# Performance work log

Hardware: AMD Instinct MI355X
Metric: run time of the kernel (lower is better)

## Reference

```python
import jax, jax.numpy as jnp
import numpy as np

N, IN, H, C, E = 20000, 256, 256, 16, 640000

def sage_conv(x, edge_index, W_l, b_l, W_r):
    # PyG SAGEConv (aggr='mean', root_weight=True):
    # out = lin_l(mean_{j in N(i)} x_j) + lin_r(x_i)
    src, dst = edge_index[0], edge_index[1]
    n = x.shape[0]
    msgs = x[src]                                            # [E, d] irregular gather
    agg = jax.ops.segment_sum(msgs, dst, num_segments=n)     # [N, d]
    deg = jax.ops.segment_sum(jnp.ones((msgs.shape[0],), x.dtype), dst, num_segments=n)
    agg = agg / jnp.maximum(deg, 1.0)[:, None]               # mean aggregation
    return agg @ W_l + b_l + x @ W_r


def setup_inputs() -> dict:
    key = jax.random.key(0)
    ks = jax.random.split(key, 10)
    s = lambda k, fi, fo: jax.random.normal(k, (fi, fo), jnp.float32) / np.sqrt(fi)
    return {
        "x": jax.random.normal(ks[0], (N, IN), jnp.float32),
        "edge_index": jax.random.randint(ks[1], (2, E), 0, N, jnp.int64),
        "W1l": s(ks[2], IN, H), "b1": jnp.zeros((H,), jnp.float32), "W1r": s(ks[3], IN, H),
        "W2l": s(ks[4], H, H),  "b2": jnp.zeros((H,), jnp.float32), "W2r": s(ks[5], H, H),
        "Wc": s(ks[6], H, C),   "bc": jnp.zeros((C,), jnp.float32),
    }


def reference(x, edge_index, W1l, b1, W1r, W2l, b2, W2r, Wc, bc):
    h = sage_conv(x, edge_index, W1l, b1, W1r)
    h = jax.nn.relu(h)                    # dropout is identity in eval mode
    z = sage_conv(h, edge_index, W2l, b2, W2r)
    return z @ Wc + bc                    # classifier logits [N, C]
```

## Files before the change

### kernel.cpp

```cpp
#include <hip/hip_runtime.h>
#include <hip/hip_bf16.h>


#define FEAT 256
#define NCLS 16
#define ZPAD 264
#define CAP  128

typedef __bf16 bf16x8 __attribute__((ext_vector_type(8)));
typedef __bf16 bf16x4 __attribute__((ext_vector_type(4)));
typedef float  f32x4  __attribute__((ext_vector_type(4)));
typedef float  f32x2  __attribute__((ext_vector_type(2)));
typedef unsigned int uint4v __attribute__((ext_vector_type(4)));

#define ACC8(S, U) do {                                                   \
    _Pragma("unroll")                                                     \
    for (int w_ = 0; w_ < 4; ++w_) {                                      \
        f32x2 lo_ = __builtin_amdgcn_cvt_pk_f32_fp8(U[w_], false);        \
        f32x2 hi_ = __builtin_amdgcn_cvt_pk_f32_fp8(U[w_], true);         \
        S[w_][0] += lo_[0]; S[w_][1] += lo_[1];                           \
        S[w_][2] += hi_[0]; S[w_][3] += hi_[1];                           \
    } } while (0)


__global__ void combo_kernel(const float* __restrict__ x,
                             const float* __restrict__ W1l, const float* __restrict__ W1r,
                             const float* __restrict__ W2l, const float* __restrict__ W2r,
                             const float* __restrict__ Wc, const float* __restrict__ b2,
                             const float* __restrict__ bc,
                             const int* __restrict__ src, const int* __restrict__ dst,
                             __bf16* __restrict__ xb, unsigned char* __restrict__ x8,
                             __bf16* __restrict__ W1lT, __bf16* __restrict__ W1rT,
                             __bf16* __restrict__ WaT, __bf16* __restrict__ WbT,
                             float* __restrict__ bc2,
                             int* __restrict__ cnt, unsigned short* __restrict__ bucket,
                             int n4, int E, int nb_edge, int nb_cvt) {
    int t = threadIdx.x;
    int bx = blockIdx.x;
    if (bx < nb_edge) {
        int e4 = (bx * 256 + t) * 4;
        if (((E & 3) == 0) && e4 + 3 < E) {
            int4 sv = *(const int4*)(src + e4);
            int4 dv = *(const int4*)(dst + e4);
            int p0 = atomicAdd(&cnt[dv.x], 1);
            int p1 = atomicAdd(&cnt[dv.y], 1);
            int p2 = atomicAdd(&cnt[dv.z], 1);
            int p3 = atomicAdd(&cnt[dv.w], 1);
            if (p0 < CAP) __builtin_nontemporal_store((unsigned short)sv.x, &bucket[(size_t)dv.x * CAP + p0]);
            if (p1 < CAP) __builtin_nontemporal_store((unsigned short)sv.y, &bucket[(size_t)dv.y * CAP + p1]);
            if (p2 < CAP) __builtin_nontemporal_store((unsigned short)sv.z, &bucket[(size_t)dv.z * CAP + p2]);
            if (p3 < CAP) __builtin_nontemporal_store((unsigned short)sv.w, &bucket[(size_t)dv.w * CAP + p3]);
        } else {
            for (int k = 0; k < 4 && e4 + k < E; ++k) {
                int s = src[e4 + k], d = dst[e4 + k];
                int p = atomicAdd(&cnt[d], 1);
                if (p < CAP) __builtin_nontemporal_store((unsigned short)s, &bucket[(size_t)d * CAP + p]);
            }
        }
    } else if (bx < nb_edge + nb_cvt) {
        int i = (bx - nb_edge) * 256 + t;
        if (i < n4) {
            f32x4 v = ((const f32x4*)x)[i];
            bf16x4 o;
            #pragma unroll
            for (int j = 0; j < 4; ++j) o[j] = (__bf16)v[j];
            ((bf16x4*)xb)[i] = o;
            int pk = 0;
            pk = __builtin_amdgcn_cvt_pk_fp8_f32(v[0], v[1], pk, false);
            pk = __builtin_amdgcn_cvt_pk_fp8_f32(v[2], v[3], pk, true);
            ((int*)x8)[i] = pk;
        }
    } else if (bx < nb_edge + nb_cvt + 512) {
        int b = bx - nb_edge - nb_cvt;
        int w = b >> 8, nn = b & 255;
        const float* W = w ? W1r : W1l;
        __bf16* WT = w ? W1rT : W1lT;
        WT[nn * FEAT + t] = (__bf16)W[t * FEAT + nn];
    } else if (bx < nb_edge + nb_cvt + 512 + 32) {
        int b = bx - nb_edge - nb_cvt - 512;
        int c = b & 15;
        const float* W = (b < 16) ? W2l : W2r;
        __bf16* WT = (b < 16) ? WaT : WbT;
        float s = 0.f;
        #pragma unroll 4
        for (int m = 0; m < FEAT; ++m)
            s += W[t * FEAT + m] * Wc[m * NCLS + c];
        WT[c * FEAT + t] = (__bf16)s;
    } else {
        if (t < NCLS) {
            float s = 0.f;
            for (int k = 0; k < FEAT; ++k) s += b2[k] * Wc[k * NCLS + t];
            bc2[t] = s + bc[t];
        }
    }
}


__global__ __launch_bounds__(256) void agg_fp8_kernel(
    const unsigned char* __restrict__ t8, const int* __restrict__ cnt,
    const unsigned short* __restrict__ bucket, __bf16* __restrict__ out, int n)
{
    int wave = threadIdx.x >> 6;
    int node = blockIdx.x * 4 + wave;
    if (node >= n) return;
    int lane = threadIdx.x & 63;
    int quad = lane >> 4, l16 = lane & 15;
    int c = cnt[node];
    int deg = c < CAP ? c : CAP;
    const unsigned short* lst = bucket + node * CAP;

    int e0 = 0, e1 = 0;
    if (lane < deg)      e0 = lst[lane];
    if (lane + 64 < deg) e1 = lst[lane + 64];

    f32x4 s0[4], s1[4];
    #pragma unroll
    for (int w = 0; w < 4; ++w) { s0[w] = (f32x4){0.f,0.f,0.f,0.f}; s1[w] = (f32x4){0.f,0.f,0.f,0.f}; }

    int nfull = deg >> 2;
    int rem   = deg & 3;
    const unsigned char* base = t8 + l16 * 16;

    int tt = 0;
    for (; tt + 3 < nfull; tt += 4) {
        int i0 = (tt + 0) * 4 + quad, i1 = (tt + 1) * 4 + quad;
        int i2 = (tt + 2) * 4 + quad, i3 = (tt + 3) * 4 + quad;
        int j0 = (i0 < 64) ? __shfl(e0, i0) : __shfl(e1, i0 - 64);
        int j1 = (i1 < 64) ? __shfl(e0, i1) : __shfl(e1, i1 - 64);
        int j2 = (i2 < 64) ? __shfl(e0, i2) : __shfl(e1, i2 - 64);
        int j3 = (i3 < 64) ? __shfl(e0, i3) : __shfl(e1, i3 - 64);
        uint4v u0 = *(const uint4v*)(base + (size_t)j0 * FEAT);
        uint4v u1 = *(const uint4v*)(base + (size_t)j1 * FEAT);
        uint4v u2 = *(const uint4v*)(base + (size_t)j2 * FEAT);
        uint4v u3 = *(const uint4v*)(base + (size_t)j3 * FEAT);
        ACC8(s0, u0); ACC8(s1, u1); ACC8(s0, u2); ACC8(s1, u3);
    }
    for (; tt < nfull; ++tt) {
        int i = tt * 4 + quad;
        int j = (i < 64) ? __shfl(e0, i) : __shfl(e1, i - 64);
        uint4v u = *(const uint4v*)(base + (size_t)j * FEAT);
        ACC8(s0, u);
    }
    if (rem) {
        int i = nfull * 4 + quad;
        int j = (i < 64) ? __shfl(e0, i) : __shfl(e1, i - 64);
        if (quad < rem) {
            uint4v u = *(const uint4v*)(base + (size_t)j * FEAT);
            ACC8(s1, u);
        }
    }

    #pragma unroll
    for (int w = 0; w < 4; ++w)
        #pragma unroll
        for (int j = 0; j < 4; ++j) {
            float v = s0[w][j] + s1[w][j];
            v += __shfl_xor(v, 16, 64);
            v += __shfl_xor(v, 32, 64);
            s0[w][j] = v;
        }

    float inv = (c > 0) ? 1.0f / (float)c : 0.0f;
    bf16x4 o;
    #pragma unroll
    for (int j = 0; j < 4; ++j) o[j] = (__bf16)(s0[quad][j] * inv);
    *(bf16x4*)(out + (size_t)node * FEAT + l16 * 16 + quad * 4) = o;
}


__global__ __launch_bounds__(256) void gemm1_kernel(
    const __bf16* __restrict__ A1, const __bf16* __restrict__ A2,
    const __bf16* __restrict__ B1T, const __bf16* __restrict__ B2T,
    const float* __restrict__ bias,
    const __bf16* __restrict__ WaT, const __bf16* __restrict__ WbT,
    const float* __restrict__ bc2,
    __bf16* __restrict__ pb, float* __restrict__ q, int M)
{
    __shared__ __align__(16) __bf16 tile[32][ZPAD];

    int m0   = blockIdx.x * 32;
    int lane = threadIdx.x & 63;
    int wave = threadIdx.x >> 6;
    int l16  = lane & 15, quad = lane >> 4;

    f32x4 acc[2][4];
    #pragma unroll
    for (int a = 0; a < 2; ++a)
        #pragma unroll
        for (int b = 0; b < 4; ++b) acc[a][b] = (f32x4){0.f, 0.f, 0.f, 0.f};

    int arow[2];
    #pragma unroll
    for (int mt = 0; mt < 2; ++mt) {
        int r = m0 + mt * 16 + l16;
        arow[mt] = (r < M) ? r : (M - 1);
    }
    int nbase = wave * 64;

    for (int pass = 0; pass < 2; ++pass) {
        const __bf16* A  = pass ? A2 : A1;
        const __bf16* BT = pass ? B2T : B1T;
        #pragma unroll 2
        for (int kk = 0; kk < 8; ++kk) {
            int k0 = kk * 32 + quad * 8;
            bf16x8 af[2], bfm[4];
            #pragma unroll
            for (int mt = 0; mt < 2; ++mt)
                af[mt] = *(const bf16x8*)(A + (size_t)arow[mt] * FEAT + k0);
            #pragma unroll
            for (int nt = 0; nt < 4; ++nt)
                bfm[nt] = *(const bf16x8*)(BT + (size_t)(nbase + nt * 16 + l16) * FEAT + k0);
            #pragma unroll
            for (int mt = 0; mt < 2; ++mt)
                #pragma unroll
                for (int nt = 0; nt < 4; ++nt)
                    acc[mt][nt] = __builtin_amdgcn_mfma_f32_16x16x32_bf16(
                        af[mt], bfm[nt], acc[mt][nt], 0, 0, 0);
        }
    }

    #pragma unroll
    for (int nt = 0; nt < 4; ++nt) {
        int col = nbase + nt * 16 + l16;
        float bv = bias[col];
        #pragma unroll
        for (int mt = 0; mt < 2; ++mt) {
            int lr = mt * 16 + quad * 4;
            #pragma unroll
            for (int r = 0; r < 4; ++r) {
                float v = acc[mt][nt][r] + bv;
                tile[lr + r][col] = (__bf16)(v > 0.f ? v : 0.f);
            }
        }
    }
    __syncthreads();

    {
        int half = wave >> 1;
        int lr = half * 16 + l16;
        const __bf16* WT = (wave & 1) ? WbT : WaT;
        f32x4 a = {0.f, 0.f, 0.f, 0.f};
        #pragma unroll
        for (int kk = 0; kk < 8; ++kk) {
            int k0 = kk * 32 + quad * 8;
            bf16x8 av = *(const bf16x8*)(&tile[lr][k0]);
            bf16x8 bv = *(const bf16x8*)(WT + (size_t)l16 * FEAT + k0);
            a = __builtin_amdgcn_mfma_f32_16x16x32_bf16(av, bv, a, 0, 0, 0);
        }
        if (wave & 1) {
            float qv = bc2[l16];
            #pragma unroll
            for (int r = 0; r < 4; ++r) {
                int row = m0 + half * 16 + quad * 4 + r;
                if (row < M) q[(size_t)row * NCLS + l16] = a[r] + qv;
            }
        } else {
            #pragma unroll
            for (int r = 0; r < 4; ++r) {
                int row = m0 + half * 16 + quad * 4 + r;
                if (row < M) pb[(size_t)row * NCLS + l16] = (__bf16)a[r];
            }
        }
    }
}


__global__ __launch_bounds__(256) void agg_out_kernel(
    const __bf16* __restrict__ pb, const float* __restrict__ q,
    const int* __restrict__ cnt, const unsigned short* __restrict__ bucket,
    float* __restrict__ out, int n)
{
    int wave = threadIdx.x >> 6;
    int node = blockIdx.x * 4 + wave;
    if (node >= n) return;
    int lane = threadIdx.x & 63;
    int quad = lane >> 4, l16 = lane & 15;
    int c = cnt[node];
    int deg = c < CAP ? c : CAP;
    const unsigned short* lst = bucket + node * CAP;

    int e0 = 0, e1 = 0;
    if (lane < deg)      e0 = lst[lane];
    if (lane + 64 < deg) e1 = lst[lane + 64];

    float s0 = 0.f, s1 = 0.f;
    int nfull = deg >> 2;
    int rem   = deg & 3;

    int tt = 0;
    for (; tt + 3 < nfull; tt += 4) {
        int i0 = (tt + 0) * 4 + quad, i1 = (tt + 1) * 4 + quad;
        int i2 = (tt + 2) * 4 + quad, i3 = (tt + 3) * 4 + quad;
        int j0 = (i0 < 64) ? __shfl(e0, i0) : __shfl(e1, i0 - 64);
        int j1 = (i1 < 64) ? __shfl(e0, i1) : __shfl(e1, i1 - 64);
        int j2 = (i2 < 64) ? __shfl(e0, i2) : __shfl(e1, i2 - 64);
        int j3 = (i3 < 64) ? __shfl(e0, i3) : __shfl(e1, i3 - 64);
        float v0 = (float)pb[(size_t)j0 * NCLS + l16];
        float v1 = (float)pb[(size_t)j1 * NCLS + l16];
        float v2 = (float)pb[(size_t)j2 * NCLS + l16];
        float v3 = (float)pb[(size_t)j3 * NCLS + l16];
        s0 += v0 + v1;
        s1 += v2 + v3;
    }
    for (; tt < nfull; ++tt) {
        int i = tt * 4 + quad;
        int j = (i < 64) ? __shfl(e0, i) : __shfl(e1, i - 64);
        s0 += (float)pb[(size_t)j * NCLS + l16];
    }
    if (rem) {
        int i = nfull * 4 + quad;
        int j = (i < 64) ? __shfl(e0, i) : __shfl(e1, i - 64);
        if (quad < rem) s1 += (float)pb[(size_t)j * NCLS + l16];
    }

    float v = s0 + s1;
    v += __shfl_xor(v, 16, 64);
    v += __shfl_xor(v, 32, 64);

    if (quad == 0) {
        float inv = (c > 0) ? 1.0f / (float)c : 0.0f;
        out[(size_t)node * NCLS + l16] = v * inv + q[(size_t)node * NCLS + l16];
    }
}


extern "C" void kernel_launch(void* const* d_in, const int* in_sizes, int n_in,
                              void* d_out, int out_size, void* d_ws, size_t ws_size,
                              hipStream_t stream) {
    const float* x   = (const float*)d_in[0];
    const int*   ei  = (const int*)d_in[1];
    const float* W1l = (const float*)d_in[2];
    const float* b1  = (const float*)d_in[3];
    const float* W1r = (const float*)d_in[4];
    const float* W2l = (const float*)d_in[5];
    const float* b2  = (const float*)d_in[6];
    const float* W2r = (const float*)d_in[7];
    const float* Wc  = (const float*)d_in[8];
    const float* bc  = (const float*)d_in[9];
    float* out = (float*)d_out;

    const int n = in_sizes[0] / FEAT;
    const int E = in_sizes[1] / 2;
    const int* srcp = ei;
    const int* dstp = ei + E;

    char* p = (char*)d_ws;
    auto alloc = [&](size_t bytes) { char* r = p; p += (bytes + 511) & ~511ull; return r; };
    int* cnt       = (int*)alloc((size_t)n * 4);
    unsigned short* bucket = (unsigned short*)alloc((size_t)n * CAP * 2);
    __bf16* W1lT   = (__bf16*)alloc((size_t)FEAT * FEAT * 2);
    __bf16* W1rT   = (__bf16*)alloc((size_t)FEAT * FEAT * 2);
    __bf16* WaT    = (__bf16*)alloc((size_t)NCLS * FEAT * 2);
    __bf16* WbT    = (__bf16*)alloc((size_t)NCLS * FEAT * 2);
    float*  bc2    = (float*)alloc((size_t)NCLS * 4);
    __bf16* xb     = (__bf16*)alloc((size_t)n * FEAT * 2);
    unsigned char* x8 = (unsigned char*)alloc((size_t)n * FEAT);
    __bf16* aggb   = (__bf16*)alloc((size_t)n * FEAT * 2);
    __bf16* pb     = (__bf16*)alloc((size_t)n * NCLS * 2);
    float*  qb     = (float*)alloc((size_t)n * NCLS * 4);

    int n4 = n * FEAT / 4;
    int nb_cvt  = (n4 + 255) / 256;
    int nb_edge = (E + 1023) / 1024;

    hipMemsetAsync(cnt, 0, (size_t)n * 4, stream);

    combo_kernel<<<nb_edge + nb_cvt + 512 + 32 + 1, 256, 0, stream>>>(
        x, W1l, W1r, W2l, W2r, Wc, b2, bc, srcp, dstp,
        xb, x8, W1lT, W1rT, WaT, WbT, bc2, cnt, bucket, n4, E, nb_edge, nb_cvt);

    agg_fp8_kernel<<<(n + 3) / 4, 256, 0, stream>>>(x8, cnt, bucket, aggb, n);
    gemm1_kernel<<<(n + 31) / 32, 256, 0, stream>>>(aggb, xb, W1lT, W1rT, b1,
                                                    WaT, WbT, bc2, pb, qb, n);

    agg_out_kernel<<<(n + 3) / 4, 256, 0, stream>>>(pb, qb, cnt, bucket, out, n);
}
```

Before: 214.0 us.

## Shard per-node edge bucket counters across eight sub-buckets to reduce atomic contention

The CSR-like bucket build now splits each destination node's counter and slot list into 8 shards chosen by block index, so concurrent atomics on the same node land on different addresses. The edge blocks move to the end of the combo kernel and handle 2 edges per thread instead of 4. The aggregation kernels rebuild a compacted neighbour list from the shard counts with a small unrolled prefix walk. In exchange, counter memory grows 8x and bucket memory 4x (larger memset and more scattered stores), and each aggregation wave does extra per-lane index arithmetic.

```diff
diff --git a/kernel.cpp b/kernel.cpp
--- a/kernel.cpp
+++ b/kernel.cpp
@@ -5,7 +5,10 @@
 #define FEAT 256
 #define NCLS 16
 #define ZPAD 264
-#define CAP  128
+#define NSH  8
+#define SCAP 64
+#define SLOTS (NSH * SCAP)
+#define CAPTOT 128
 
 typedef __bf16 bf16x8 __attribute__((ext_vector_type(8)));
 typedef __bf16 bf16x4 __attribute__((ext_vector_type(4)));
@@ -21,6 +24,36 @@
         S[w_][0] += lo_[0]; S[w_][1] += lo_[1];                           \
         S[w_][2] += hi_[0]; S[w_][3] += hi_[1];                           \
     } } while (0)
+
+__device__ __forceinline__ void load_entries(
+    const int* __restrict__ cnt, const unsigned short* __restrict__ bucket,
+    int node, int lane, int& e0, int& e1, int& deg, float& inv)
+{
+    int4 ca = *(const int4*)(cnt + node * NSH);
+    int4 cb = *(const int4*)(cnt + node * NSH + 4);
+    int cs[NSH] = {ca.x, ca.y, ca.z, ca.w, cb.x, cb.y, cb.z, cb.w};
+    int ctrue = 0, d = 0;
+    #pragma unroll
+    for (int s = 0; s < NSH; ++s) {
+        ctrue += cs[s];
+        cs[s] = cs[s] < SCAP ? cs[s] : SCAP;
+        d += cs[s];
+    }
+    deg = d < CAPTOT ? d : CAPTOT;
+    inv = ctrue > 0 ? 1.0f / (float)ctrue : 0.0f;
+    const unsigned short* lst = bucket + (size_t)node * SLOTS;
+
+    auto get = [&](int i) -> int {
+        int s = 0, loc = i;
+        #pragma unroll
+        for (int t = 0; t < NSH - 1; ++t) {
+            if (s == t && loc >= cs[t]) { loc -= cs[t]; s = t + 1; }
+        }
+        return lst[s * SCAP + loc];
+    };
+    e0 = (lane < deg)      ? get(lane)      : 0;
+    e1 = (lane + 64 < deg) ? get(lane + 64) : 0;
+}
 
 
 __global__ void combo_kernel(const float* __restrict__ x,
@@ -34,31 +67,11 @@
                              __bf16* __restrict__ WaT, __bf16* __restrict__ WbT,
                              float* __restrict__ bc2,
                              int* __restrict__ cnt, unsigned short* __restrict__ bucket,
-                             int n4, int E, int nb_edge, int nb_cvt) {
+                             int n4, int E, int nb_cvt) {
     int t = threadIdx.x;
     int bx = blockIdx.x;
-    if (bx < nb_edge) {
-        int e4 = (bx * 256 + t) * 4;
-        if (((E & 3) == 0) && e4 + 3 < E) {
-            int4 sv = *(const int4*)(src + e4);
-            int4 dv = *(const int4*)(dst + e4);
-            int p0 = atomicAdd(&cnt[dv.x], 1);
-            int p1 = atomicAdd(&cnt[dv.y], 1);
-            int p2 = atomicAdd(&cnt[dv.z], 1);
-            int p3 = atomicAdd(&cnt[dv.w], 1);
-            if (p0 < CAP) __builtin_nontemporal_store((unsigned short)sv.x, &bucket[(size_t)dv.x * CAP + p0]);
-            if (p1 < CAP) __builtin_nontemporal_store((unsigned short)sv.y, &bucket[(size_t)dv.y * CAP + p1]);
-            if (p2 < CAP) __builtin_nontemporal_store((unsigned short)sv.z, &bucket[(size_t)dv.z * CAP + p2]);
-            if (p3 < CAP) __builtin_nontemporal_store((unsigned short)sv.w, &bucket[(size_t)dv.w * CAP + p3]);
-        } else {
-            for (int k = 0; k < 4 && e4 + k < E; ++k) {
-                int s = src[e4 + k], d = dst[e4 + k];
-                int p = atomicAdd(&cnt[d], 1);
-                if (p < CAP) __builtin_nontemporal_store((unsigned short)s, &bucket[(size_t)d * CAP + p]);
-            }
-        }
-    } else if (bx < nb_edge + nb_cvt) {
-        int i = (bx - nb_edge) * 256 + t;
+    if (bx < nb_cvt) {
+        int i = bx * 256 + t;
         if (i < n4) {
             f32x4 v = ((const f32x4*)x)[i];
             bf16x4 o;
@@ -70,14 +83,14 @@
             pk = __builtin_amdgcn_cvt_pk_fp8_f32(v[2], v[3], pk, true);
             ((int*)x8)[i] = pk;
         }
-    } else if (bx < nb_edge + nb_cvt + 512) {
-        int b = bx - nb_edge - nb_cvt;
+    } else if (bx < nb_cvt + 512) {
+        int b = bx - nb_cvt;
         int w = b >> 8, nn = b & 255;
         const float* W = w ? W1r : W1l;
         __bf16* WT = w ? W1rT : W1lT;
         WT[nn * FEAT + t] = (__bf16)W[t * FEAT + nn];
-    } else if (bx < nb_edge + nb_cvt + 512 + 32) {
-        int b = bx - nb_edge - nb_cvt - 512;
+    } else if (bx < nb_cvt + 512 + 32) {
+        int b = bx - nb_cvt - 512;
         int c = b & 15;
         const float* W = (b < 16) ? W2l : W2r;
         __bf16* WT = (b < 16) ? WaT : WbT;
@@ -86,11 +99,25 @@
         for (int m = 0; m < FEAT; ++m)
             s += W[t * FEAT + m] * Wc[m * NCLS + c];
         WT[c * FEAT + t] = (__bf16)s;
-    } else {
+    } else if (bx == nb_cvt + 512 + 32) {
         if (t < NCLS) {
             float s = 0.f;
             for (int k = 0; k < FEAT; ++k) s += b2[k] * Wc[k * NCLS + t];
             bc2[t] = s + bc[t];
+        }
+    } else {
+        int sh = bx & (NSH - 1);
+        int idx = (bx - nb_cvt - 512 - 33) * 256 + t;
+        int e2 = idx * 2;
+        if (e2 < E) {
+            int2 sv = *(const int2*)(src + e2);
+            int2 dv = *(const int2*)(dst + e2);
+            int p0 = atomicAdd(&cnt[dv.x * NSH + sh], 1);
+            if (p0 < SCAP) bucket[(size_t)dv.x * SLOTS + sh * SCAP + p0] = (unsigned short)sv.x;
+            if (e2 + 1 < E) {
+                int p1 = atomicAdd(&cnt[dv.y * NSH + sh], 1);
+                if (p1 < SCAP) bucket[(size_t)dv.y * SLOTS + sh * SCAP + p1] = (unsigned short)sv.y;
+            }
         }
     }
 }
@@ -105,13 +132,9 @@
     if (node >= n) return;
     int lane = threadIdx.x & 63;
     int quad = lane >> 4, l16 = lane & 15;
-    int c = cnt[node];
-    int deg = c < CAP ? c : CAP;
-    const unsigned short* lst = bucket + node * CAP;
-
-    int e0 = 0, e1 = 0;
-    if (lane < deg)      e0 = lst[lane];
-    if (lane + 64 < deg) e1 = lst[lane + 64];
+
+    int e0, e1, deg; float inv;
+    load_entries(cnt, bucket, node, lane, e0, e1, deg, inv);
 
     f32x4 s0[4], s1[4];
     #pragma unroll
@@ -160,7 +183,6 @@
             s0[w][j] = v;
         }
 
-    float inv = (c > 0) ? 1.0f / (float)c : 0.0f;
     bf16x4 o;
     #pragma unroll
     for (int j = 0; j < 4; ++j) o[j] = (__bf16)(s0[quad][j] * inv);
@@ -275,13 +297,9 @@
     if (node >= n) return;
     int lane = threadIdx.x & 63;
     int quad = lane >> 4, l16 = lane & 15;
-    int c = cnt[node];
-    int deg = c < CAP ? c : CAP;
-    const unsigned short* lst = bucket + node * CAP;
-
-    int e0 = 0, e1 = 0;
-    if (lane < deg)      e0 = lst[lane];
-    if (lane + 64 < deg) e1 = lst[lane + 64];
+
+    int e0, e1, deg; float inv;
+    load_entries(cnt, bucket, node, lane, e0, e1, deg, inv);
 
     float s0 = 0.f, s1 = 0.f;
     int nfull = deg >> 2;
@@ -318,7 +336,6 @@
     v += __shfl_xor(v, 32, 64);
 
     if (quad == 0) {
-        float inv = (c > 0) ? 1.0f / (float)c : 0.0f;
         out[(size_t)node * NCLS + l16] = v * inv + q[(size_t)node * NCLS + l16];
     }
 }
@@ -346,8 +363,8 @@
 
     char* p = (char*)d_ws;
     auto alloc = [&](size_t bytes) { char* r = p; p += (bytes + 511) & ~511ull; return r; };
-    int* cnt       = (int*)alloc((size_t)n * 4);
-    unsigned short* bucket = (unsigned short*)alloc((size_t)n * CAP * 2);
+    int* cnt       = (int*)alloc((size_t)n * NSH * 4);
+    unsigned short* bucket = (unsigned short*)alloc((size_t)n * SLOTS * 2);
     __bf16* W1lT   = (__bf16*)alloc((size_t)FEAT * FEAT * 2);
     __bf16* W1rT   = (__bf16*)alloc((size_t)FEAT * FEAT * 2);
     __bf16* WaT    = (__bf16*)alloc((size_t)NCLS * FEAT * 2);
@@ -361,13 +378,13 @@
 
     int n4 = n * FEAT / 4;
     int nb_cvt  = (n4 + 255) / 256;
-    int nb_edge = (E + 1023) / 1024;
-
-    hipMemsetAsync(cnt, 0, (size_t)n * 4, stream);
-
-    combo_kernel<<<nb_edge + nb_cvt + 512 + 32 + 1, 256, 0, stream>>>(
+    int nb_edge = (E + 511) / 512;
+
+    hipMemsetAsync(cnt, 0, (size_t)n * NSH * 4, stream);
+
+    combo_kernel<<<nb_cvt + 512 + 32 + 1 + nb_edge, 256, 0, stream>>>(
         x, W1l, W1r, W2l, W2r, Wc, b2, bc, srcp, dstp,
-        xb, x8, W1lT, W1rT, WaT, WbT, bc2, cnt, bucket, n4, E, nb_edge, nb_cvt);
+        xb, x8, W1lT, W1rT, WaT, WbT, bc2, cnt, bucket, n4, E, nb_cvt);
 
     agg_fp8_kernel<<<(n + 3) / 4, 256, 0, stream>>>(x8, cnt, bucket, aggb, n);
     gemm1_kernel<<<(n + 31) / 32, 256, 0, stream>>>(aggb, xb, W1lT, W1rT, b1,
```

After: 195.7 us. 1.09x faster.
